# Kernel optimization log

Hardware: AMD Instinct MI355X
Metric: run time of the kernel (lower is better)

The kernel has to match this reference:

```python
import jax, jax.numpy as jnp
import numpy as np

N_QUBITS = 12
R = 1
EDGES = [(i, (i + 1) % N_QUBITS) for i in range(N_QUBITS)]
DIM = 2 ** N_QUBITS
BATCH = 64
_LET = 'abcdefghijklmnopqrstuvwxy'

_I4 = np.eye(4, dtype=np.float32)
_AD = np.fliplr(_I4).copy()                      # antidiagonal (XX imag pattern)
_YP = np.array([[0,0,0,1],[0,0,-1,0],[0,-1,0,0],[1,0,0,0]], dtype=np.float32)  # YY imag pattern
_CNOT = jnp.asarray(np.array([[1,0,0,0],[0,1,0,0],[0,0,0,1],[0,0,1,0]], dtype=np.complex64))
_k = np.arange(DIM)
# z_signs[i, k] = -1 if bit (n-i-1) of k is set, matching the torch buffer
_ZS = jnp.asarray(np.stack([1.0 - 2.0 * ((_k >> (N_QUBITS - i - 1)) & 1) for i in range(N_QUBITS)]).astype(np.float32))  # [n, 2^n]


def _c(r, i):
    return jax.lax.complex(r, i)


def rx_mat(t):
    c, s, z = jnp.cos(t / 2), jnp.sin(t / 2), jnp.zeros_like(t)
    real = jnp.stack([jnp.stack([c, z], -1), jnp.stack([z, c], -1)], -2)
    imag = jnp.stack([jnp.stack([z, -s], -1), jnp.stack([-s, z], -1)], -2)
    return _c(real, imag)


def ry_mat(t):
    c, s = jnp.cos(t / 2), jnp.sin(t / 2)
    real = jnp.stack([jnp.stack([c, -s], -1), jnp.stack([s, c], -1)], -2)
    return _c(real, jnp.zeros_like(real))


def rz_mat(t):
    p, z = t / 2, jnp.zeros_like(t)
    cp, sp = jnp.cos(p), jnp.sin(p)
    real = jnp.stack([jnp.stack([cp, z], -1), jnp.stack([z, cp], -1)], -2)
    imag = jnp.stack([jnp.stack([-sp, z], -1), jnp.stack([z, sp], -1)], -2)
    return _c(real, imag)


def ising_zz(t):
    p = t / 2
    c, s = jnp.cos(p), jnp.sin(p)
    dr = jnp.stack([c, c, c, c], -1)
    di = jnp.stack([-s, s, s, -s], -1)
    i4 = jnp.asarray(_I4)
    return _c(dr[..., :, None] * i4, di[..., :, None] * i4)


def ising_xx(t):
    c, s = jnp.cos(t / 2), jnp.sin(t / 2)
    return _c(c[..., None, None] * jnp.asarray(_I4), -s[..., None, None] * jnp.asarray(_AD))


def ising_yy(t):
    c, s = jnp.cos(t / 2), jnp.sin(t / 2)
    return _c(c[..., None, None] * jnp.asarray(_I4), s[..., None, None] * jnp.asarray(_YP))


def apply_1q(state, gate, q):
    # state [B, 2^n]; gate [2,2] or [B,2,2]; qubit axis sits at stride 2^q (matches torch view)
    B = state.shape[0]
    left, right = 2 ** (N_QUBITS - q - 1), 2 ** q
    s = state.reshape(B, left, 2, right)
    sub = 'bij' if gate.ndim == 3 else 'ij'
    return jnp.einsum(f'{sub},bljr->blir', gate, s).reshape(B, DIM)


def apply_2q(state, gate, q1, q2):
    # state [B, 2^n]; gate [4,4]; qubit index = tensor-axis index from MSB (matches torch permute path)
    if q1 > q2:
        q1, q2 = q2, q1
    B = state.shape[0]
    s = state.reshape((B,) + (2,) * N_QUBITS)
    g = gate.reshape(2, 2, 2, 2)
    ax = list(_LET[:N_QUBITS])
    out = ax.copy()
    u, v = ax[q1], ax[q2]
    out[q1], out[q2] = 'A', 'B'
    spec = f"AB{u}{v},Z{''.join(ax)}->Z{''.join(out)}"
    return jnp.einsum(spec, g, s).reshape(B, DIM)


def _forward(data, encoding_scale, encoding_bias, eta, ew_zz, ew_xx, ew_yy, nb_z, nb_x, nb_y, trainable_rots):
    B, n = data.shape
    # data-encoding gates, cached once per forward: angles [B, n] -> gates [B, n, 2, 2]
    rx_g = rx_mat(encoding_scale[:, 0] * data + encoding_bias[:, 0])
    ry_g = ry_mat(encoding_scale[:, 1] * data + encoding_bias[:, 1])
    rz_g = rz_mat(encoding_scale[:, 2] * data + encoding_bias[:, 2])
    state = jnp.zeros((B, DIM), jnp.complex64).at[:, 0].set(1.0)
    ising_fns = (ising_zz, ising_xx, ising_yy)
    ews = (ew_zz, ew_xx, ew_yy)
    nbs = (nb_z, nb_x, nb_y)
    bias_fns = (rz_mat, rx_mat, ry_mat)
    enc_types = ('full', 'xy', 'yz')
    for r in range(R):
        for b in range(3):  # blocks: ZZ, XX, YY
            bt = enc_types[b]
            # data encoding
            for q in range(n):
                if bt != 'yz':
                    state = apply_1q(state, rx_g[:, q], q)
                state = apply_1q(state, ry_g[:, q], q)
                if bt != 'xy':
                    state = apply_1q(state, rz_g[:, q], q)
            # Ising interaction on each edge
            theta = eta[r, b] * ews[b][r]            # [n_edges]
            egs = ising_fns[b](theta)                # [n_edges, 4, 4]
            for e, (i, j) in enumerate(EDGES):
                state = apply_2q(state, egs[e], i, j)
            # node biases (RZ / RX / RY matching the block)
            bgs = bias_fns[b](nbs[b][r])             # [n, 2, 2]
            for q in range(n):
                state = apply_1q(state, bgs[q], q)
            # trainable rotations rx, ry, rz per qubit
            rots = trainable_rots[r, b]              # [n, 3]
            rxg, ryg, rzg = rx_mat(rots[:, 0]), ry_mat(rots[:, 1]), rz_mat(rots[:, 2])
            for q in range(n):
                state = apply_1q(state, rxg[q], q)
                state = apply_1q(state, ryg[q], q)
                state = apply_1q(state, rzg[q], q)
            # CNOT entangling ring
            for q in range(n):
                state = apply_2q(state, _CNOT, q, (q + 1) % n)
    probs = state.real ** 2 + state.imag ** 2        # [B, 2^n]
    return probs @ _ZS.T                             # Pauli-Z expectations [B, n]


def setup_inputs() -> dict:
    key = jax.random.key(0)
    ks = jax.random.split(key, 12)
    n, E, f = N_QUBITS, len(EDGES), jnp.float32
    return {
        'data': jax.random.uniform(ks[0], (BATCH, n), f),
        'encoding_scale': jnp.pi * jnp.ones((n, 3), f) + 0.1 * jax.random.normal(ks[1], (n, 3), f),
        'encoding_bias': 0.1 * jax.random.normal(ks[2], (n, 3), f),
        'eta': 0.5 * jnp.ones((R, 3), f),
        'ew_zz': jnp.ones((R, E), f) + 0.1 * jax.random.normal(ks[3], (R, E), f),
        'ew_xx': jnp.ones((R, E), f) + 0.1 * jax.random.normal(ks[4], (R, E), f),
        'ew_yy': jnp.ones((R, E), f) + 0.1 * jax.random.normal(ks[5], (R, E), f),
        'nb_z': 0.1 * jax.random.normal(ks[6], (R, n), f),
        'nb_x': 0.1 * jax.random.normal(ks[7], (R, n), f),
        'nb_y': 0.1 * jax.random.normal(ks[8], (R, n), f),
        'trainable_rots': 0.1 * jax.random.normal(ks[9], (R, 3, n, 3), f),
    }


def reference(data, encoding_scale, encoding_bias, eta, ew_zz, ew_xx, ew_yy, nb_z, nb_x, nb_y, trainable_rots):
    return _forward(data, encoding_scale, encoding_bias, eta, ew_zz, ew_xx, ew_yy, nb_z, nb_x, nb_y, trainable_rots)
```

## Files before the change

kernel.cpp:

```cpp
#include <hip/hip_runtime.h>
#include <math.h>

#define NT 512
#define QDIM 4096

using F2 = float2;

__device__ __forceinline__ F2 cadd(F2 p, F2 q) { return make_float2(p.x + q.x, p.y + q.y); }
__device__ __forceinline__ F2 cmul(F2 p, F2 q) {
    return make_float2(p.x * q.x - p.y * q.y, p.x * q.y + p.y * q.x);
}

struct M2 { F2 a, b, c, d; };

__device__ __forceinline__ M2 mmul(M2 A, M2 B) {
    M2 R;
    R.a = cadd(cmul(A.a, B.a), cmul(A.b, B.c));
    R.b = cadd(cmul(A.a, B.b), cmul(A.b, B.d));
    R.c = cadd(cmul(A.c, B.a), cmul(A.d, B.c));
    R.d = cadd(cmul(A.c, B.b), cmul(A.d, B.d));
    return R;
}

__device__ __forceinline__ M2 mrx(float t) {
    float s, c; sincosf(0.5f * t, &s, &c);
    return { make_float2(c, 0), make_float2(0, -s), make_float2(0, -s), make_float2(c, 0) };
}
__device__ __forceinline__ M2 mry(float t) {
    float s, c; sincosf(0.5f * t, &s, &c);
    return { make_float2(c, 0), make_float2(-s, 0), make_float2(s, 0), make_float2(c, 0) };
}
__device__ __forceinline__ M2 mrz(float t) {
    float s, c; sincosf(0.5f * t, &s, &c);
    return { make_float2(c, -s), make_float2(0, 0), make_float2(0, 0), make_float2(c, s) };
}

#define RSQ2 0.70710678118654752f
__device__ __forceinline__ M2 mH() {
    return { make_float2(RSQ2, 0), make_float2(RSQ2, 0), make_float2(RSQ2, 0), make_float2(-RSQ2, 0) };
}
__device__ __forceinline__ M2 mW() {
    return { make_float2(RSQ2, 0), make_float2(0, RSQ2), make_float2(RSQ2, 0), make_float2(0, -RSQ2) };
}
__device__ __forceinline__ M2 mWd() {
    return { make_float2(RSQ2, 0), make_float2(RSQ2, 0), make_float2(0, -RSQ2), make_float2(0, RSQ2) };
}


template<int JB>
__device__ __forceinline__ void g1_reg(F2* amp, const F2* g) {
    const int m = 1 << JB;
    F2 m00 = g[0], m01 = g[1], m10 = g[2], m11 = g[3];
#pragma unroll
    for (int j = 0; j < 8; ++j)
        if (!(j & m)) {
            F2 a = amp[j], b = amp[j | m];
            amp[j]     = cadd(cmul(m00, a), cmul(m01, b));
            amp[j | m] = cadd(cmul(m10, a), cmul(m11, b));
        }
}

template<int LM>
__device__ __forceinline__ void g1_shfl(F2* amp, const F2* g, int lane) {
    bool u = (lane & LM) != 0;
    F2 gs = u ? g[3] : g[0];
    F2 gp = u ? g[2] : g[1];
#pragma unroll
    for (int j = 0; j < 8; ++j) {
        F2 p;
        p.x = __shfl_xor(amp[j].x, LM, 64);
        p.y = __shfl_xor(amp[j].y, LM, 64);
        amp[j] = cadd(cmul(gs, amp[j]), cmul(gp, p));
    }
}

__device__ __forceinline__ void swap_to_Lp(F2* amp, int tid, int l, int w, F2* b) {
#pragma unroll
    for (int j = 0; j < 8; ++j) b[j * 512 + tid] = amp[j];
    __syncthreads();
#pragma unroll
    for (int j = 0; j < 8; ++j) amp[j] = b[w * 512 + (j << 6) + l];
}

__device__ __forceinline__ void swap_to_L0(F2* amp, int tid, int l, int w, F2* b) {
#pragma unroll
    for (int j = 0; j < 8; ++j) b[w * 512 + (j << 6) + l] = amp[j];
    __syncthreads();
#pragma unroll
    for (int j = 0; j < 8; ++j) amp[j] = b[j * 512 + tid];
}

__device__ __forceinline__ void diag_all_Lp(F2* amp, const float* zhalf, int l, int w) {
    float zr[12];
#pragma unroll
    for (int e = 0; e < 12; ++e) zr[e] = zhalf[e];
#pragma unroll
    for (int j = 0; j < 8; ++j) {
        int k = (j << 9) | (l << 3) | w;
        float phi = 0.f;
#pragma unroll
        for (int e = 0; e < 12; ++e) {
            int hi = (e < 11) ? 11 - e : 11, lo = (e < 11) ? 10 - e : 0;
            phi += (((k >> hi) ^ (k >> lo)) & 1) ? zr[e] : -zr[e];
        }
        float sp, cp;
        __sincosf(phi, &sp, &cp);
        amp[j] = cmul(amp[j], make_float2(cp, sp));
    }
}

__device__ __forceinline__ int cnot_src(int k) {
#pragma unroll
    for (int e = 11; e >= 0; --e) {
        int hi = (e < 11) ? 11 - e : 11, lo = (e < 11) ? 10 - e : 0;
        if ((k >> hi) & 1) k ^= (1 << lo);
    }
    return k;
}

__device__ __forceinline__ void cnot_trip(F2* amp, int tid, const int* kslot, F2* b) {
#pragma unroll
    for (int j = 0; j < 8; ++j) b[j * 512 + tid] = amp[j];
    __syncthreads();
#pragma unroll
    for (int j = 0; j < 8; ++j) amp[j] = b[kslot[j]];
}

__global__ __launch_bounds__(NT) void qsim_kernel(
    const float* __restrict__ data,
    const float* __restrict__ enc_scale,
    const float* __restrict__ enc_bias,
    const float* __restrict__ eta,
    const float* __restrict__ ew_zz,
    const float* __restrict__ ew_xx,
    const float* __restrict__ ew_yy,
    const float* __restrict__ nb_z,
    const float* __restrict__ nb_x,
    const float* __restrict__ nb_y,
    const float* __restrict__ trots,
    float* __restrict__ out)
{
    __shared__ F2 buf[2][QDIM];
    __shared__ F2 g1q[72][4];
    __shared__ float zhalf[3][12];
    __shared__ float red[8][12];

    const int tid = threadIdx.x;
    const int l = tid & 63, w = tid >> 6;
    const int bat = blockIdx.x;

    if (tid < 36) {
        int b = tid / 12, q = tid % 12;
        float x  = data[bat * 12 + q];
        float ax = enc_scale[q * 3 + 0] * x + enc_bias[q * 3 + 0];
        float ay = enc_scale[q * 3 + 1] * x + enc_bias[q * 3 + 1];
        float az = enc_scale[q * 3 + 2] * x + enc_bias[q * 3 + 2];
        M2 M;
        if (b == 0)      M = mmul(mrz(az), mmul(mry(ay), mrx(ax)));
        else if (b == 1) M = mmul(mH(), mmul(mry(ay), mrx(ax)));
        else             M = mmul(mW(), mmul(mrz(az), mry(ay)));
        g1q[tid][0] = M.a; g1q[tid][1] = M.b; g1q[tid][2] = M.c; g1q[tid][3] = M.d;
    } else if (tid < 72) {
        int i = tid - 36, b = i / 12, q = i % 12;
        float nb = (b == 0) ? nb_z[q] : (b == 1) ? nb_x[q] : nb_y[q];
        M2 M0 = (b == 0) ? mrz(nb) : (b == 1) ? mrx(nb) : mry(nb);
        float t0 = trots[(b * 12 + q) * 3 + 0];
        float t1 = trots[(b * 12 + q) * 3 + 1];
        float t2 = trots[(b * 12 + q) * 3 + 2];
        M2 M = mmul(mrz(t2), mmul(mry(t1), mmul(mrx(t0), M0)));
        if (b == 1)      M = mmul(M, mH());
        else if (b == 2) M = mmul(M, mWd());
        g1q[tid][0] = M.a; g1q[tid][1] = M.b; g1q[tid][2] = M.c; g1q[tid][3] = M.d;
    } else if (tid < 108) {
        int i = tid - 72, b = i / 12, e = i % 12;
        const float* ew = (b == 0) ? ew_zz : (b == 1) ? ew_xx : ew_yy;
        zhalf[b][e] = 0.5f * eta[b] * ew[e];
    }
    __syncthreads();

    F2 amp[8];
#pragma unroll
    for (int j = 0; j < 8; ++j) amp[j] = make_float2(0.f, 0.f);
    if (tid == 0) amp[0].x = 1.f;

    int kslot[8];
#pragma unroll
    for (int j = 0; j < 8; ++j) {
        int ks = cnot_src((tid << 3) | j);
        kslot[j] = (ks & 7) * 512 + (ks >> 3);
    }

    int sel = 0;
#define NB (&buf[(sel ^= 1) ^ 1][0])

    for (int blk = 0; blk < 3; ++blk) {
        const F2(*Ge)[4] = &g1q[blk * 12];
        const F2(*Gb)[4] = &g1q[36 + blk * 12];

        g1_reg<0>(amp, Ge[0]);  g1_reg<1>(amp, Ge[1]);  g1_reg<2>(amp, Ge[2]);
        g1_shfl<1>(amp, Ge[3], l);  g1_shfl<2>(amp, Ge[4], l);  g1_shfl<4>(amp, Ge[5], l);
        g1_shfl<8>(amp, Ge[6], l);  g1_shfl<16>(amp, Ge[7], l); g1_shfl<32>(amp, Ge[8], l);
        swap_to_Lp(amp, tid, l, w, NB);
        g1_reg<0>(amp, Ge[9]);  g1_reg<1>(amp, Ge[10]);  g1_reg<2>(amp, Ge[11]);

        diag_all_Lp(amp, zhalf[blk], l, w);

        g1_reg<0>(amp, Gb[9]);  g1_reg<1>(amp, Gb[10]);  g1_reg<2>(amp, Gb[11]);
        g1_shfl<1>(amp, Gb[3], l);  g1_shfl<2>(amp, Gb[4], l);  g1_shfl<4>(amp, Gb[5], l);
        g1_shfl<8>(amp, Gb[6], l);  g1_shfl<16>(amp, Gb[7], l); g1_shfl<32>(amp, Gb[8], l);
        swap_to_L0(amp, tid, l, w, NB);
        g1_reg<0>(amp, Gb[0]);  g1_reg<1>(amp, Gb[1]);  g1_reg<2>(amp, Gb[2]);

        cnot_trip(amp, tid, kslot, NB);
    }

    float acc[12];
#pragma unroll
    for (int i = 0; i < 12; ++i) acc[i] = 0.f;
#pragma unroll
    for (int j = 0; j < 8; ++j) {
        int k = (tid << 3) | j;
        float pr = amp[j].x * amp[j].x + amp[j].y * amp[j].y;
#pragma unroll
        for (int i = 0; i < 12; ++i)
            acc[i] += ((k >> (11 - i)) & 1) ? -pr : pr;
    }
#pragma unroll
    for (int off = 32; off > 0; off >>= 1)
#pragma unroll
        for (int i = 0; i < 12; ++i)
            acc[i] += __shfl_down(acc[i], off, 64);
    int wv = tid >> 6;
    if ((tid & 63) == 0)
#pragma unroll
        for (int i = 0; i < 12; ++i) red[wv][i] = acc[i];
    __syncthreads();
    if (tid < 12) {
        float s = 0.f;
#pragma unroll
        for (int ww = 0; ww < 8; ++ww) s += red[ww][tid];
        out[bat * 12 + tid] = s;
    }
}

extern "C" void kernel_launch(void* const* d_in, const int* in_sizes, int n_in,
                              void* d_out, int out_size, void* d_ws, size_t ws_size,
                              hipStream_t stream) {
    const float* data      = (const float*)d_in[0];
    const float* enc_scale = (const float*)d_in[1];
    const float* enc_bias  = (const float*)d_in[2];
    const float* eta       = (const float*)d_in[3];
    const float* ew_zz     = (const float*)d_in[4];
    const float* ew_xx     = (const float*)d_in[5];
    const float* ew_yy     = (const float*)d_in[6];
    const float* nb_z      = (const float*)d_in[7];
    const float* nb_x      = (const float*)d_in[8];
    const float* nb_y      = (const float*)d_in[9];
    const float* trots     = (const float*)d_in[10];
    float* out = (float*)d_out;

    int batch = out_size / 12;
    qsim_kernel<<<batch, NT, 0, stream>>>(data, enc_scale, enc_bias, eta,
                                          ew_zz, ew_xx, ew_yy,
                                          nb_z, nb_x, nb_y, trots, out);
}
```

Measured before the change: 106.2 us.

## Replace shuffle-based gates with LDS transposes across four register layouts

Drops the per-gate wavefront shuffles for middle qubits. Each block now cycles the state through four layouts via shared-memory transposes (trips), so every gate becomes an in-register butterfly. Shared-memory stores use an XOR swizzle to avoid bank conflicts. The diagonal phase and the final Z-expectation reduction are simplified for the new layout. The cost is more LDS round trips and barriers per block (six plus the CNOT permutation, instead of two plus one).

```diff
diff --git a/kernel.cpp b/kernel.cpp
--- a/kernel.cpp
+++ b/kernel.cpp
@@ -47,6 +47,28 @@
 }
 
 
+template<int Li>
+__device__ __forceinline__ int kOf(int t, int j) {
+    const int mlo = (1 << (3 * Li)) - 1;
+    return (t & mlo) | (j << (3 * Li)) | ((t & ~mlo) << 3);
+}
+template<int Li>
+__device__ __forceinline__ int slotOf(int k) {
+    const int mlo = (1 << (3 * Li)) - 1;
+    int j = (k >> (3 * Li)) & 7;
+    int t = (k & mlo) | ((k >> 3) & ~mlo);
+    return j * 512 + (t ^ j);
+}
+
+template<int LA, int LB>
+__device__ __forceinline__ void trip(F2* amp, int tid, F2* b) {
+#pragma unroll
+    for (int j = 0; j < 8; ++j) b[j * 512 + (tid ^ j)] = amp[j];
+    __syncthreads();
+#pragma unroll
+    for (int j = 0; j < 8; ++j) amp[j] = b[slotOf<LA>(kOf<LB>(tid, j))];
+}
+
 template<int JB>
 __device__ __forceinline__ void g1_reg(F2* amp, const F2* g) {
     const int m = 1 << JB;
@@ -60,49 +82,23 @@
         }
 }
 
-template<int LM>
-__device__ __forceinline__ void g1_shfl(F2* amp, const F2* g, int lane) {
-    bool u = (lane & LM) != 0;
-    F2 gs = u ? g[3] : g[0];
-    F2 gp = u ? g[2] : g[1];
+__device__ __forceinline__ void diag_L3(F2* amp, const float* zh, int tid) {
+    float phi0 = 0.f;
+#pragma unroll
+    for (int e = 3; e <= 10; ++e) {
+        int hi = 11 - e, lo = 10 - e;
+        phi0 += (((tid >> hi) ^ (tid >> lo)) & 1) ? zh[e] : -zh[e];
+    }
+    float z0 = zh[0], z1 = zh[1], z2 = zh[2], z11 = zh[11];
+    int t8 = (tid >> 8) & 1, t0 = tid & 1;
 #pragma unroll
     for (int j = 0; j < 8; ++j) {
-        F2 p;
-        p.x = __shfl_xor(amp[j].x, LM, 64);
-        p.y = __shfl_xor(amp[j].y, LM, 64);
-        amp[j] = cadd(cmul(gs, amp[j]), cmul(gp, p));
-    }
-}
-
-__device__ __forceinline__ void swap_to_Lp(F2* amp, int tid, int l, int w, F2* b) {
-#pragma unroll
-    for (int j = 0; j < 8; ++j) b[j * 512 + tid] = amp[j];
-    __syncthreads();
-#pragma unroll
-    for (int j = 0; j < 8; ++j) amp[j] = b[w * 512 + (j << 6) + l];
-}
-
-__device__ __forceinline__ void swap_to_L0(F2* amp, int tid, int l, int w, F2* b) {
-#pragma unroll
-    for (int j = 0; j < 8; ++j) b[w * 512 + (j << 6) + l] = amp[j];
-    __syncthreads();
-#pragma unroll
-    for (int j = 0; j < 8; ++j) amp[j] = b[j * 512 + tid];
-}
-
-__device__ __forceinline__ void diag_all_Lp(F2* amp, const float* zhalf, int l, int w) {
-    float zr[12];
-#pragma unroll
-    for (int e = 0; e < 12; ++e) zr[e] = zhalf[e];
-#pragma unroll
-    for (int j = 0; j < 8; ++j) {
-        int k = (j << 9) | (l << 3) | w;
-        float phi = 0.f;
-#pragma unroll
-        for (int e = 0; e < 12; ++e) {
-            int hi = (e < 11) ? 11 - e : 11, lo = (e < 11) ? 10 - e : 0;
-            phi += (((k >> hi) ^ (k >> lo)) & 1) ? zr[e] : -zr[e];
-        }
+        int j0 = j & 1, j1 = (j >> 1) & 1, j2 = (j >> 2) & 1;
+        float phi = phi0
+            + ((j2 ^ j1) ? z0 : -z0)
+            + ((j1 ^ j0) ? z1 : -z1)
+            + ((j0 ^ t8) ? z2 : -z2)
+            + ((j2 ^ t0) ? z11 : -z11);
         float sp, cp;
         __sincosf(phi, &sp, &cp);
         amp[j] = cmul(amp[j], make_float2(cp, sp));
@@ -120,7 +116,7 @@
 
 __device__ __forceinline__ void cnot_trip(F2* amp, int tid, const int* kslot, F2* b) {
 #pragma unroll
-    for (int j = 0; j < 8; ++j) b[j * 512 + tid] = amp[j];
+    for (int j = 0; j < 8; ++j) b[j * 512 + (tid ^ j)] = amp[j];
     __syncthreads();
 #pragma unroll
     for (int j = 0; j < 8; ++j) amp[j] = b[kslot[j]];
@@ -146,7 +142,6 @@
     __shared__ float red[8][12];
 
     const int tid = threadIdx.x;
-    const int l = tid & 63, w = tid >> 6;
     const int bat = blockIdx.x;
 
     if (tid < 36) {
@@ -185,10 +180,8 @@
 
     int kslot[8];
 #pragma unroll
-    for (int j = 0; j < 8; ++j) {
-        int ks = cnot_src((tid << 3) | j);
-        kslot[j] = (ks & 7) * 512 + (ks >> 3);
-    }
+    for (int j = 0; j < 8; ++j)
+        kslot[j] = slotOf<0>(cnot_src(kOf<0>(tid, j)));
 
     int sel = 0;
 #define NB (&buf[(sel ^= 1) ^ 1][0])
@@ -198,32 +191,45 @@
         const F2(*Gb)[4] = &g1q[36 + blk * 12];
 
         g1_reg<0>(amp, Ge[0]);  g1_reg<1>(amp, Ge[1]);  g1_reg<2>(amp, Ge[2]);
-        g1_shfl<1>(amp, Ge[3], l);  g1_shfl<2>(amp, Ge[4], l);  g1_shfl<4>(amp, Ge[5], l);
-        g1_shfl<8>(amp, Ge[6], l);  g1_shfl<16>(amp, Ge[7], l); g1_shfl<32>(amp, Ge[8], l);
-        swap_to_Lp(amp, tid, l, w, NB);
-        g1_reg<0>(amp, Ge[9]);  g1_reg<1>(amp, Ge[10]);  g1_reg<2>(amp, Ge[11]);
-
-        diag_all_Lp(amp, zhalf[blk], l, w);
-
-        g1_reg<0>(amp, Gb[9]);  g1_reg<1>(amp, Gb[10]);  g1_reg<2>(amp, Gb[11]);
-        g1_shfl<1>(amp, Gb[3], l);  g1_shfl<2>(amp, Gb[4], l);  g1_shfl<4>(amp, Gb[5], l);
-        g1_shfl<8>(amp, Gb[6], l);  g1_shfl<16>(amp, Gb[7], l); g1_shfl<32>(amp, Gb[8], l);
-        swap_to_L0(amp, tid, l, w, NB);
+        trip<0,1>(amp, tid, NB);
+        g1_reg<0>(amp, Ge[3]);  g1_reg<1>(amp, Ge[4]);  g1_reg<2>(amp, Ge[5]);
+        trip<1,2>(amp, tid, NB);
+        g1_reg<0>(amp, Ge[6]);  g1_reg<1>(amp, Ge[7]);  g1_reg<2>(amp, Ge[8]);
+        trip<2,3>(amp, tid, NB);
+        g1_reg<0>(amp, Ge[9]);  g1_reg<1>(amp, Ge[10]); g1_reg<2>(amp, Ge[11]);
+
+        diag_L3(amp, zhalf[blk], tid);
+
+        g1_reg<0>(amp, Gb[9]);  g1_reg<1>(amp, Gb[10]); g1_reg<2>(amp, Gb[11]);
+        trip<3,2>(amp, tid, NB);
+        g1_reg<0>(amp, Gb[6]);  g1_reg<1>(amp, Gb[7]);  g1_reg<2>(amp, Gb[8]);
+        trip<2,1>(amp, tid, NB);
+        g1_reg<0>(amp, Gb[3]);  g1_reg<1>(amp, Gb[4]);  g1_reg<2>(amp, Gb[5]);
+        trip<1,0>(amp, tid, NB);
         g1_reg<0>(amp, Gb[0]);  g1_reg<1>(amp, Gb[1]);  g1_reg<2>(amp, Gb[2]);
 
         cnot_trip(amp, tid, kslot, NB);
     }
 
+    float pr[8];
+#pragma unroll
+    for (int j = 0; j < 8; ++j) pr[j] = amp[j].x * amp[j].x + amp[j].y * amp[j].y;
+    float psum = 0.f;
+#pragma unroll
+    for (int j = 0; j < 8; ++j) psum += pr[j];
+
     float acc[12];
 #pragma unroll
-    for (int i = 0; i < 12; ++i) acc[i] = 0.f;
-#pragma unroll
-    for (int j = 0; j < 8; ++j) {
-        int k = (tid << 3) | j;
-        float pr = amp[j].x * amp[j].x + amp[j].y * amp[j].y;
-#pragma unroll
-        for (int i = 0; i < 12; ++i)
-            acc[i] += ((k >> (11 - i)) & 1) ? -pr : pr;
+    for (int i = 0; i < 9; ++i)
+        acc[i] = ((tid >> (8 - i)) & 1) ? -psum : psum;
+#pragma unroll
+    for (int i = 9; i < 12; ++i) {
+        float s = 0.f;
+        int bit = 11 - i;
+#pragma unroll
+        for (int j = 0; j < 8; ++j)
+            s += ((j >> bit) & 1) ? -pr[j] : pr[j];
+        acc[i] = s;
     }
 #pragma unroll
     for (int off = 32; off > 0; off >>= 1)
```

Measured after the change: 103.3 us. 1.03x faster.
